# Performance work log

Hardware: AMD Instinct MI355X
Metric: run time of the kernel (lower is better)

The kernel has to match this reference:

```python
import jax, jax.numpy as jnp
import numpy as np

B, T, V = 128, 257, 1024   # T = U + 1 (structural constraint of the module)
U = 256
N_EMB, D_EMB = 1000, 512
NEG = -1e30
BLANK = 0


def setup_inputs() -> dict:
    key = jax.random.key(0)
    k0, k1, k2, k3, k4 = jax.random.split(key, 5)
    x = jax.random.normal(k0, (B, T, V), jnp.float32)
    y = jax.random.randint(k1, (B, U), 1, N_EMB, dtype=jnp.int32)  # labels in [1, 999], never blank
    xlen = jnp.full((B,), T, jnp.int32)
    ylen = jnp.full((B,), U, jnp.int32)
    embed_w = jax.random.normal(k2, (N_EMB, D_EMB), jnp.float32)
    lin_w = jax.random.normal(k3, (V, D_EMB), jnp.float32) / np.float32(np.sqrt(D_EMB))
    lin_b = jax.random.normal(k4, (V,), jnp.float32) * 0.01
    return {"x": x, "xlen": xlen, "y": y, "ylen": ylen,
            "embed_w": embed_w, "lin_w": lin_w, "lin_b": lin_b}


def _ctc_loss_sum(lp, targets, xlen, ylen):
    # lp: [T, B, V] treated as log-probs (faithful to the original, which feeds raw
    # logits straight into torch.nn.CTCLoss). targets: [B, U] padded with blank.
    Tn, Bn, _ = lp.shape
    Un = targets.shape[1]
    S = 2 * Un + 1
    # extended label sequence: blank, y1, blank, y2, ..., blank   -> [B, S]
    ext = jnp.full((Bn, S), BLANK, targets.dtype).at[:, 1::2].set(targets)
    bidx = jnp.arange(Bn)[:, None]
    lp_ext = lp[:, bidx, ext]                       # [T, B, S]
    # skip transition s-2 -> s allowed iff ext[s] != blank and ext[s] != ext[s-2]
    ext_m2 = jnp.pad(ext, ((0, 0), (2, 0)), constant_values=-1)[:, :S]
    skip_ok = (ext != BLANK) & (ext != ext_m2)      # [B, S]

    def lse3(a, b, c):
        m = jnp.maximum(jnp.maximum(a, b), c)
        return m + jnp.log(jnp.exp(a - m) + jnp.exp(b - m) + jnp.exp(c - m))

    alpha0 = (jnp.full((Bn, S), NEG, lp.dtype)
              .at[:, 0].set(lp_ext[0, :, 0])
              .at[:, 1].set(lp_ext[0, :, 1]))

    def step(alpha, lp_t):
        a1 = jnp.pad(alpha, ((0, 0), (1, 0)), constant_values=NEG)[:, :S]
        a2 = jnp.pad(alpha, ((0, 0), (2, 0)), constant_values=NEG)[:, :S]
        a2 = jnp.where(skip_ok, a2, NEG)
        new = lp_t + lse3(alpha, a1, a2)
        return new, new

    _, rest = jax.lax.scan(step, alpha0, lp_ext[1:])
    alphas = jnp.concatenate([alpha0[None], rest], axis=0)   # [T, B, S]
    aT = alphas[xlen - 1, jnp.arange(Bn)]                    # [B, S] at each seq's last frame
    s_last = 2 * ylen                                        # final blank position
    ll = jnp.logaddexp(aT[jnp.arange(Bn), s_last],
                       aT[jnp.arange(Bn), s_last - 1])
    return -jnp.sum(ll)                                      # reduction='sum'


def reference(x, xlen, y, ylen, embed_w, lin_w, lin_b):
    # mask padded label positions to blank (make_pad_mask + masked_fill_)
    pad = jnp.arange(y.shape[1], dtype=ylen.dtype)[None, :] >= ylen[:, None]
    y = jnp.where(pad, 0, y)
    z = jnp.concatenate([jnp.zeros((y.shape[0], 1), y.dtype), y], axis=1)  # [B, U+1]
    h = embed_w[z]                                   # [B, T, 512]
    logits = x + h @ lin_w.T + lin_b                 # [B, T, 1024]
    log_probs = jnp.transpose(logits, (1, 0, 2))     # [T, B, V]
    return _ctc_loss_sum(log_probs, y, xlen, ylen)
```

## Files before the change

kernel.cpp:

```cpp
#include <hip/hip_runtime.h>

#define NEG (-1e30f)

constexpr int B_ = 128;
constexpr int T_ = 257;
constexpr int V_ = 1024;
constexpr int U_ = 256;
constexpr int DE_ = 512;


__global__ __launch_bounds__(256) void gather_kernel(const float* __restrict__ x,
                                                     const int* __restrict__ y,
                                                     const int* __restrict__ ylen,
                                                     const float* __restrict__ E,
                                                     const float* __restrict__ L,
                                                     const float* __restrict__ bias,
                                                     float4* __restrict__ V)
{
    const int wave = (blockIdx.x << 2) | (threadIdx.x >> 6);
    if (wave >= B_ * T_) return;
    const int lane = threadIdx.x & 63;
    const int t = wave >> 7;
    const int b = wave & 127;

    const int yl = ylen[b];
    int ym1 = 0, yt = 0, ym2 = 0;
    if (t >= 1 && (t - 1) < yl) ym1 = y[b * U_ + t - 1];
    if (t <= 255 && t < yl)     yt  = y[b * U_ + t];
    if (t >= 2 && (t - 2) < yl) ym2 = y[b * U_ + t - 2];
    const int z = (t == 0) ? 0 : ym1;

    const float4* Ez = (const float4*)(E + (size_t)z * DE_);
    const float4* L0 = (const float4*)L;
    const float4* Lz = (const float4*)(L + (size_t)z * DE_);
    const float4* Lh = (const float4*)(L + (size_t)yt * DE_);
    float s_bl = 0.f, s_lo = 0.f, s_hi = 0.f;
    #pragma unroll
    for (int h = 0; h < 2; ++h) {
        const int idx = lane + h * 64;
        const float4 e = Ez[idx];
        const float4 l0 = L0[idx], lz = Lz[idx], lh = Lh[idx];
        s_bl += e.x * l0.x + e.y * l0.y + e.z * l0.z + e.w * l0.w;
        s_lo += e.x * lz.x + e.y * lz.y + e.z * lz.z + e.w * lz.w;
        s_hi += e.x * lh.x + e.y * lh.y + e.z * lh.z + e.w * lh.w;
    }
    #pragma unroll
    for (int m = 1; m < 64; m <<= 1) {
        s_bl += __shfl_xor(s_bl, m, 64);
        s_lo += __shfl_xor(s_lo, m, 64);
        s_hi += __shfl_xor(s_hi, m, 64);
    }

    if (lane == 0) {
        const float* xrow = x + ((size_t)b * T_ + t) * V_;
        const float v_bl = xrow[0] + s_bl + bias[0];
        const float v_lo = (t >= 1) ? (xrow[z] + s_lo + bias[z]) : NEG;
        const float v_hi = xrow[yt] + s_hi + bias[yt];
        int flags = 0;
        if (t >= 1 && t <= 255 && yt != 0 && yt != ym1) flags |= 1;
        if (t >= 2 && ym1 != 0 && ym1 != ym2)           flags |= 2;
        V[wave] = make_float4(v_lo, v_bl, v_hi, __int_as_float(flags));
    }
}

__global__ __launch_bounds__(128) void ctc_band_kernel(const float4* __restrict__ V,
                                                       float* __restrict__ out)
{
    const int tid = threadIdx.x;

    float4 ring[8];
    #pragma unroll
    for (int i = 0; i < 8; ++i) ring[i] = V[i * B_ + tid];

    float lo = NEG, mid = ring[0].y, hi = ring[0].z;
    ring[0] = V[8 * B_ + tid];

    for (int tb = 0; tb < 32; ++tb) {
        #pragma unroll
        for (int j = 1; j <= 8; ++j) {
            const int t = tb * 8 + j;
            const float4 f = ring[j & 7];
            if (t + 8 <= 256) ring[j & 7] = V[(size_t)(t + 8) * B_ + tid];
            const int flags = __float_as_int(f.w);
            const float nh = f.z + ((flags & 1) ? hi : NEG);
            const float nm = f.y + hi;
            const float a2 = (flags & 2) ? lo : NEG;
            const float m = fmaxf(fmaxf(hi, mid), a2);
            const float nl = f.x + m +
                __logf(__expf(hi - m) + __expf(mid - m) + __expf(a2 - m));
            hi = nh; mid = nm; lo = nl;
        }
    }
    const float mm = fmaxf(mid, lo);
    const float ll = mm + __logf(__expf(mid - mm) + __expf(lo - mm));

    __shared__ float sh[B_];
    sh[tid] = ll;
    __syncthreads();
    if (tid < 64) {
        float v = sh[tid] + sh[tid + 64];
        #pragma unroll
        for (int m = 1; m < 64; m <<= 1) v += __shfl_xor(v, m, 64);
        if (tid == 0) out[0] = -v;
    }
}

extern "C" void kernel_launch(void* const* d_in, const int* in_sizes, int n_in,
                              void* d_out, int out_size, void* d_ws, size_t ws_size,
                              hipStream_t stream)
{
    const float* x       = (const float*)d_in[0];
    const int*   y       = (const int*)  d_in[2];
    const int*   ylen    = (const int*)  d_in[3];
    const float* embed_w = (const float*)d_in[4];
    const float* lin_w   = (const float*)d_in[5];
    const float* lin_b   = (const float*)d_in[6];

    float4* V = (float4*)d_ws;
    float* out = (float*)d_out;

    const int n_tasks = B_ * T_;
    gather_kernel<<<dim3((n_tasks + 3) / 4), dim3(256), 0, stream>>>(
        x, y, ylen, embed_w, lin_w, lin_b, V);
    ctc_band_kernel<<<dim3(1), dim3(128), 0, stream>>>(V, out);
}
```

Baseline: 235.9 us.

## Fuse gather and CTC recursion into one kernel via last-block atomic counter

Merges the per-frame gather kernel and the single-block CTC alpha recursion into one launch. Each block bumps a global atomic counter after writing its results, and the last block to finish runs the serial band recursion and the final reduction. The x-row loads are also issued earlier, before the dot products. This removes one kernel launch and its inter-kernel gap, at the cost of a memset of the counter and a fence plus atomic in every block.

```diff
diff --git a/kernel.cpp b/kernel.cpp
--- a/kernel.cpp
+++ b/kernel.cpp
@@ -7,95 +7,111 @@
 constexpr int V_ = 1024;
 constexpr int U_ = 256;
 constexpr int DE_ = 512;
+constexpr int NWAVE_ = B_ * T_;
+constexpr int NBLK_ = (NWAVE_ + 3) / 4;
 
-
-__global__ __launch_bounds__(256) void gather_kernel(const float* __restrict__ x,
-                                                     const int* __restrict__ y,
-                                                     const int* __restrict__ ylen,
-                                                     const float* __restrict__ E,
-                                                     const float* __restrict__ L,
-                                                     const float* __restrict__ bias,
-                                                     float4* __restrict__ V)
+__global__ __launch_bounds__(256) void fused_ctc_kernel(const float* __restrict__ x,
+                                                        const int* __restrict__ y,
+                                                        const int* __restrict__ ylen,
+                                                        const float* __restrict__ E,
+                                                        const float* __restrict__ L,
+                                                        const float* __restrict__ bias,
+                                                        float4* __restrict__ V,
+                                                        unsigned* __restrict__ cnt,
+                                                        float* __restrict__ out)
 {
     const int wave = (blockIdx.x << 2) | (threadIdx.x >> 6);
-    if (wave >= B_ * T_) return;
     const int lane = threadIdx.x & 63;
-    const int t = wave >> 7;
-    const int b = wave & 127;
+    if (wave < NWAVE_) {
+        const int t = wave >> 7;
+        const int b = wave & 127;
 
-    const int yl = ylen[b];
-    int ym1 = 0, yt = 0, ym2 = 0;
-    if (t >= 1 && (t - 1) < yl) ym1 = y[b * U_ + t - 1];
-    if (t <= 255 && t < yl)     yt  = y[b * U_ + t];
-    if (t >= 2 && (t - 2) < yl) ym2 = y[b * U_ + t - 2];
-    const int z = (t == 0) ? 0 : ym1;
+        const int yl = ylen[b];
+        int ym1 = 0, yt = 0, ym2 = 0;
+        if (t >= 1 && (t - 1) < yl) ym1 = y[b * U_ + t - 1];
+        if (t <= 255 && t < yl)     yt  = y[b * U_ + t];
+        if (t >= 2 && (t - 2) < yl) ym2 = y[b * U_ + t - 2];
+        const int z = (t == 0) ? 0 : ym1;
 
-    const float4* Ez = (const float4*)(E + (size_t)z * DE_);
-    const float4* L0 = (const float4*)L;
-    const float4* Lz = (const float4*)(L + (size_t)z * DE_);
-    const float4* Lh = (const float4*)(L + (size_t)yt * DE_);
-    float s_bl = 0.f, s_lo = 0.f, s_hi = 0.f;
-    #pragma unroll
-    for (int h = 0; h < 2; ++h) {
-        const int idx = lane + h * 64;
-        const float4 e = Ez[idx];
-        const float4 l0 = L0[idx], lz = Lz[idx], lh = Lh[idx];
-        s_bl += e.x * l0.x + e.y * l0.y + e.z * l0.z + e.w * l0.w;
-        s_lo += e.x * lz.x + e.y * lz.y + e.z * lz.z + e.w * lz.w;
-        s_hi += e.x * lh.x + e.y * lh.y + e.z * lh.z + e.w * lh.w;
-    }
-    #pragma unroll
-    for (int m = 1; m < 64; m <<= 1) {
-        s_bl += __shfl_xor(s_bl, m, 64);
-        s_lo += __shfl_xor(s_lo, m, 64);
-        s_hi += __shfl_xor(s_hi, m, 64);
+        const float* xrow = x + ((size_t)b * T_ + t) * V_;
+        const float xb0 = xrow[0];
+        const float xbz = xrow[z];
+        const float xbh = xrow[yt];
+
+        const float4* Ez = (const float4*)(E + (size_t)z * DE_);
+        const float4* L0 = (const float4*)L;
+        const float4* Lz = (const float4*)(L + (size_t)z * DE_);
+        const float4* Lh = (const float4*)(L + (size_t)yt * DE_);
+        float s_bl = 0.f, s_lo = 0.f, s_hi = 0.f;
+        #pragma unroll
+        for (int h = 0; h < 2; ++h) {
+            const int idx = lane + h * 64;
+            const float4 e = Ez[idx];
+            const float4 l0 = L0[idx], lz = Lz[idx], lh = Lh[idx];
+            s_bl += e.x * l0.x + e.y * l0.y + e.z * l0.z + e.w * l0.w;
+            s_lo += e.x * lz.x + e.y * lz.y + e.z * lz.z + e.w * lz.w;
+            s_hi += e.x * lh.x + e.y * lh.y + e.z * lh.z + e.w * lh.w;
+        }
+        #pragma unroll
+        for (int m = 1; m < 64; m <<= 1) {
+            s_bl += __shfl_xor(s_bl, m, 64);
+            s_lo += __shfl_xor(s_lo, m, 64);
+            s_hi += __shfl_xor(s_hi, m, 64);
+        }
+
+        if (lane == 0) {
+            const float v_bl = xb0 + s_bl + bias[0];
+            const float v_lo = (t >= 1) ? (xbz + s_lo + bias[z]) : NEG;
+            const float v_hi = xbh + s_hi + bias[yt];
+            int flags = 0;
+            if (t >= 1 && t <= 255 && yt != 0 && yt != ym1) flags |= 1;
+            if (t >= 2 && ym1 != 0 && ym1 != ym2)           flags |= 2;
+            V[wave] = make_float4(v_lo, v_bl, v_hi, __int_as_float(flags));
+        }
     }
 
-    if (lane == 0) {
-        const float* xrow = x + ((size_t)b * T_ + t) * V_;
-        const float v_bl = xrow[0] + s_bl + bias[0];
-        const float v_lo = (t >= 1) ? (xrow[z] + s_lo + bias[z]) : NEG;
-        const float v_hi = xrow[yt] + s_hi + bias[yt];
-        int flags = 0;
-        if (t >= 1 && t <= 255 && yt != 0 && yt != ym1) flags |= 1;
-        if (t >= 2 && ym1 != 0 && ym1 != ym2)           flags |= 2;
-        V[wave] = make_float4(v_lo, v_bl, v_hi, __int_as_float(flags));
+    __shared__ int is_last;
+    __syncthreads();
+    if (threadIdx.x == 0) {
+        __threadfence();
+        is_last = (atomicAdd(cnt, 1u) == (unsigned)(NBLK_ - 1));
     }
-}
+    __syncthreads();
+    if (!is_last) return;
+    __threadfence();
 
-__global__ __launch_bounds__(128) void ctc_band_kernel(const float4* __restrict__ V,
-                                                       float* __restrict__ out)
-{
     const int tid = threadIdx.x;
+    float ll = 0.f;
+    if (tid < B_) {
+        float4 ring[8];
+        #pragma unroll
+        for (int i = 0; i < 8; ++i) ring[i] = V[i * B_ + tid];
 
-    float4 ring[8];
-    #pragma unroll
-    for (int i = 0; i < 8; ++i) ring[i] = V[i * B_ + tid];
+        float lo = NEG, mid = ring[0].y, hi = ring[0].z;
+        ring[0] = V[8 * B_ + tid];
 
-    float lo = NEG, mid = ring[0].y, hi = ring[0].z;
-    ring[0] = V[8 * B_ + tid];
-
-    for (int tb = 0; tb < 32; ++tb) {
-        #pragma unroll
-        for (int j = 1; j <= 8; ++j) {
-            const int t = tb * 8 + j;
-            const float4 f = ring[j & 7];
-            if (t + 8 <= 256) ring[j & 7] = V[(size_t)(t + 8) * B_ + tid];
-            const int flags = __float_as_int(f.w);
-            const float nh = f.z + ((flags & 1) ? hi : NEG);
-            const float nm = f.y + hi;
-            const float a2 = (flags & 2) ? lo : NEG;
-            const float m = fmaxf(fmaxf(hi, mid), a2);
-            const float nl = f.x + m +
-                __logf(__expf(hi - m) + __expf(mid - m) + __expf(a2 - m));
-            hi = nh; mid = nm; lo = nl;
+        for (int tb = 0; tb < 32; ++tb) {
+            #pragma unroll
+            for (int j = 1; j <= 8; ++j) {
+                const int t = tb * 8 + j;
+                const float4 f = ring[j & 7];
+                if (t + 8 <= 256) ring[j & 7] = V[(size_t)(t + 8) * B_ + tid];
+                const int flags = __float_as_int(f.w);
+                const float nh = f.z + ((flags & 1) ? hi : NEG);
+                const float nm = f.y + hi;
+                const float a2 = (flags & 2) ? lo : NEG;
+                const float m = fmaxf(fmaxf(hi, mid), a2);
+                const float nl = f.x + m +
+                    __logf(__expf(hi - m) + __expf(mid - m) + __expf(a2 - m));
+                hi = nh; mid = nm; lo = nl;
+            }
         }
+        const float mm = fmaxf(mid, lo);
+        ll = mm + __logf(__expf(mid - mm) + __expf(lo - mm));
     }
-    const float mm = fmaxf(mid, lo);
-    const float ll = mm + __logf(__expf(mid - mm) + __expf(lo - mm));
 
     __shared__ float sh[B_];
-    sh[tid] = ll;
+    if (tid < B_) sh[tid] = ll;
     __syncthreads();
     if (tid < 64) {
         float v = sh[tid] + sh[tid + 64];
@@ -116,11 +132,11 @@
     const float* lin_w   = (const float*)d_in[5];
     const float* lin_b   = (const float*)d_in[6];
 
-    float4* V = (float4*)d_ws;
-    float* out = (float*)d_out;
+    float4*   V   = (float4*)d_ws;
+    unsigned* cnt = (unsigned*)((char*)d_ws + (size_t)NWAVE_ * sizeof(float4));
+    float*    out = (float*)d_out;
 
-    const int n_tasks = B_ * T_;
-    gather_kernel<<<dim3((n_tasks + 3) / 4), dim3(256), 0, stream>>>(
-        x, y, ylen, embed_w, lin_w, lin_b, V);
-    ctc_band_kernel<<<dim3(1), dim3(128), 0, stream>>>(V, out);
+    hipMemsetAsync(cnt, 0, sizeof(unsigned), stream);
+    fused_ctc_kernel<<<dim3(NBLK_), dim3(256), 0, stream>>>(
+        x, y, ylen, embed_w, lin_w, lin_b, V, cnt, out);
 }
```

New measurement: 472.7 us. +100.3%, slower.

## Stream CTC scan inputs through LDS with async global_load_lds and hoist x loads

Applied to the files above, without the earlier changes.

The serial CTC scan kernel now prefetches per-timestep float4 records into a 4-slot LDS ring with global_load_lds, three chunks of 8 timesteps ahead, and waits with an explicit vmcnt. This replaces the 8-deep register ring, aiming to hide global latency on the single-block critical path. The gather kernel issues its x-row loads before the dot-product reduction so their latency overlaps the arithmetic. It also reads past T for padded chunks (up to t=282 rows), which may read beyond the written workspace region, though those values are unused.

```diff
diff --git a/kernel.cpp b/kernel.cpp
--- a/kernel.cpp
+++ b/kernel.cpp
@@ -7,6 +7,13 @@
 constexpr int V_ = 1024;
 constexpr int U_ = 256;
 constexpr int DE_ = 512;
+constexpr int NWAVE_ = B_ * T_;
+constexpr int TPAD_ = 280;
+
+#define GLOAD_LDS(g, l)                                                     \
+    __builtin_amdgcn_global_load_lds(                                       \
+        (const __attribute__((address_space(1))) void*)(g),                 \
+        (__attribute__((address_space(3))) void*)(l), 16, 0, 0)
 
 
 __global__ __launch_bounds__(256) void gather_kernel(const float* __restrict__ x,
@@ -18,7 +25,7 @@
                                                      float4* __restrict__ V)
 {
     const int wave = (blockIdx.x << 2) | (threadIdx.x >> 6);
-    if (wave >= B_ * T_) return;
+    if (wave >= NWAVE_) return;
     const int lane = threadIdx.x & 63;
     const int t = wave >> 7;
     const int b = wave & 127;
@@ -29,6 +36,11 @@
     if (t <= 255 && t < yl)     yt  = y[b * U_ + t];
     if (t >= 2 && (t - 2) < yl) ym2 = y[b * U_ + t - 2];
     const int z = (t == 0) ? 0 : ym1;
+
+    const float* xrow = x + ((size_t)b * T_ + t) * V_;
+    const float xb0 = xrow[0];
+    const float xbz = xrow[z];
+    const float xbh = xrow[yt];
 
     const float4* Ez = (const float4*)(E + (size_t)z * DE_);
     const float4* L0 = (const float4*)L;
@@ -52,10 +64,9 @@
     }
 
     if (lane == 0) {
-        const float* xrow = x + ((size_t)b * T_ + t) * V_;
-        const float v_bl = xrow[0] + s_bl + bias[0];
-        const float v_lo = (t >= 1) ? (xrow[z] + s_lo + bias[z]) : NEG;
-        const float v_hi = xrow[yt] + s_hi + bias[yt];
+        const float v_bl = xb0 + s_bl + bias[0];
+        const float v_lo = (t >= 1) ? (xbz + s_lo + bias[z]) : NEG;
+        const float v_hi = xbh + s_hi + bias[yt];
         int flags = 0;
         if (t >= 1 && t <= 255 && yt != 0 && yt != ym1) flags |= 1;
         if (t >= 2 && ym1 != 0 && ym1 != ym2)           flags |= 2;
@@ -63,46 +74,75 @@
     }
 }
 
-__global__ __launch_bounds__(128) void ctc_band_kernel(const float4* __restrict__ V,
+__global__ __launch_bounds__(128) void ctc_scan_kernel(const float4* __restrict__ V,
                                                        float* __restrict__ out)
 {
+    __shared__ __align__(16) float buf[2][4][8][256];
     const int tid = threadIdx.x;
+    const int w = tid >> 6;
+    const int lane = tid & 63;
 
-    float4 ring[8];
+    const float4* gbase = V + w * 64 + lane;
+
     #pragma unroll
-    for (int i = 0; i < 8; ++i) ring[i] = V[i * B_ + tid];
+    for (int c = 0; c < 3; ++c)
+        #pragma unroll
+        for (int r = 0; r < 8; ++r)
+            GLOAD_LDS(gbase + (size_t)(c * 8 + r) * B_, &buf[w][c][r][0]);
 
-    float lo = NEG, mid = ring[0].y, hi = ring[0].z;
-    ring[0] = V[8 * B_ + tid];
+    asm volatile("s_waitcnt vmcnt(16)" ::: "memory");
 
-    for (int tb = 0; tb < 32; ++tb) {
+    float lo = NEG, mid, hi;
+    {
+        const float4 f = *(const float4*)&buf[w][0][0][lane * 4];
+        mid = f.y; hi = f.z;
+    }
+    #pragma unroll
+    for (int r = 1; r < 8; ++r) {
+        const float4 f = *(const float4*)&buf[w][0][r][lane * 4];
+        const int flags = __float_as_int(f.w);
+        const float nh = f.z + ((flags & 1) ? hi : NEG);
+        const float nm = f.y + hi;
+        const float a2 = (flags & 2) ? lo : NEG;
+        const float m = fmaxf(fmaxf(hi, mid), a2);
+        const float nl = f.x + m +
+            __logf(__expf(hi - m) + __expf(mid - m) + __expf(a2 - m));
+        hi = nh; mid = nm; lo = nl;
+    }
+
+    for (int c = 1; c <= 32; ++c) {
+        const int snew = (c + 2) & 3;
         #pragma unroll
-        for (int j = 1; j <= 8; ++j) {
-            const int t = tb * 8 + j;
-            const float4 f = ring[j & 7];
-            if (t + 8 <= 256) ring[j & 7] = V[(size_t)(t + 8) * B_ + tid];
-            const int flags = __float_as_int(f.w);
-            const float nh = f.z + ((flags & 1) ? hi : NEG);
-            const float nm = f.y + hi;
-            const float a2 = (flags & 2) ? lo : NEG;
-            const float m = fmaxf(fmaxf(hi, mid), a2);
-            const float nl = f.x + m +
-                __logf(__expf(hi - m) + __expf(mid - m) + __expf(a2 - m));
-            hi = nh; mid = nm; lo = nl;
+        for (int r = 0; r < 8; ++r)
+            GLOAD_LDS(gbase + (size_t)((c + 2) * 8 + r) * B_, &buf[w][snew][r][0]);
+        asm volatile("s_waitcnt vmcnt(16)" ::: "memory");
+        const int slot = c & 3;
+        #pragma unroll
+        for (int r = 0; r < 8; ++r) {
+            const int t = c * 8 + r;
+            if (t <= 256) {
+                const float4 f = *(const float4*)&buf[w][slot][r][lane * 4];
+                const int flags = __float_as_int(f.w);
+                const float nh = f.z + ((flags & 1) ? hi : NEG);
+                const float nm = f.y + hi;
+                const float a2 = (flags & 2) ? lo : NEG;
+                const float m = fmaxf(fmaxf(hi, mid), a2);
+                const float nl = f.x + m +
+                    __logf(__expf(hi - m) + __expf(mid - m) + __expf(a2 - m));
+                hi = nh; mid = nm; lo = nl;
+            }
         }
     }
+
     const float mm = fmaxf(mid, lo);
-    const float ll = mm + __logf(__expf(mid - mm) + __expf(lo - mm));
+    float ll = mm + __logf(__expf(mid - mm) + __expf(lo - mm));
+    #pragma unroll
+    for (int m = 1; m < 64; m <<= 1) ll += __shfl_xor(ll, m, 64);
 
-    __shared__ float sh[B_];
-    sh[tid] = ll;
     __syncthreads();
-    if (tid < 64) {
-        float v = sh[tid] + sh[tid + 64];
-        #pragma unroll
-        for (int m = 1; m < 64; m <<= 1) v += __shfl_xor(v, m, 64);
-        if (tid == 0) out[0] = -v;
-    }
+    if (lane == 0) ((volatile float*)buf)[w] = ll;
+    __syncthreads();
+    if (tid == 0) out[0] = -(((volatile float*)buf)[0] + ((volatile float*)buf)[1]);
 }
 
 extern "C" void kernel_launch(void* const* d_in, const int* in_sizes, int n_in,
@@ -116,11 +156,11 @@
     const float* lin_w   = (const float*)d_in[5];
     const float* lin_b   = (const float*)d_in[6];
 
-    float4* V = (float4*)d_ws;
+    float4* V  = (float4*)d_ws;
     float* out = (float*)d_out;
 
-    const int n_tasks = B_ * T_;
-    gather_kernel<<<dim3((n_tasks + 3) / 4), dim3(256), 0, stream>>>(
+    const int nblk = (NWAVE_ + 3) / 4;
+    gather_kernel<<<dim3(nblk), dim3(256), 0, stream>>>(
         x, y, ylen, embed_w, lin_w, lin_b, V);
-    ctc_band_kernel<<<dim3(1), dim3(128), 0, stream>>>(V, out);
+    ctc_scan_kernel<<<dim3(1), dim3(128), 0, stream>>>(V, out);
 }
```

After: 228.8 us. 1.03x faster.

## Split CTC scan across eight blocks with LDS staging and atomic reduction

Applied to the files above, without the earlier changes.

Splits the serial CTC recurrence from one 128-thread block into eight blocks, each handling 16 batch items. The gather kernel now writes in a group-major layout so each block can bulk-load its 256 timesteps into shared memory before a 16-lane scan reads them from LDS instead of global memory. The per-group partial sums are combined with an atomicAdd onto an output zeroed by a memset. The x-row loads are also issued before the dot products to overlap their latency. This spreads the latency-bound scan over more compute units, at the cost of an extra memset launch and a nondeterministic float summation order.

```diff
diff --git a/kernel.cpp b/kernel.cpp
--- a/kernel.cpp
+++ b/kernel.cpp
@@ -7,6 +7,7 @@
 constexpr int V_ = 1024;
 constexpr int U_ = 256;
 constexpr int DE_ = 512;
+constexpr int NWAVE_ = B_ * T_;
 
 
 __global__ __launch_bounds__(256) void gather_kernel(const float* __restrict__ x,
@@ -18,7 +19,7 @@
                                                      float4* __restrict__ V)
 {
     const int wave = (blockIdx.x << 2) | (threadIdx.x >> 6);
-    if (wave >= B_ * T_) return;
+    if (wave >= NWAVE_) return;
     const int lane = threadIdx.x & 63;
     const int t = wave >> 7;
     const int b = wave & 127;
@@ -29,6 +30,11 @@
     if (t <= 255 && t < yl)     yt  = y[b * U_ + t];
     if (t >= 2 && (t - 2) < yl) ym2 = y[b * U_ + t - 2];
     const int z = (t == 0) ? 0 : ym1;
+
+    const float* xrow = x + ((size_t)b * T_ + t) * V_;
+    const float xb0 = xrow[0];
+    const float xbz = xrow[z];
+    const float xbh = xrow[yt];
 
     const float4* Ez = (const float4*)(E + (size_t)z * DE_);
     const float4* L0 = (const float4*)L;
@@ -52,35 +58,39 @@
     }
 
     if (lane == 0) {
-        const float* xrow = x + ((size_t)b * T_ + t) * V_;
-        const float v_bl = xrow[0] + s_bl + bias[0];
-        const float v_lo = (t >= 1) ? (xrow[z] + s_lo + bias[z]) : NEG;
-        const float v_hi = xrow[yt] + s_hi + bias[yt];
+        const float v_bl = xb0 + s_bl + bias[0];
+        const float v_lo = (t >= 1) ? (xbz + s_lo + bias[z]) : NEG;
+        const float v_hi = xbh + s_hi + bias[yt];
         int flags = 0;
         if (t >= 1 && t <= 255 && yt != 0 && yt != ym1) flags |= 1;
         if (t >= 2 && ym1 != 0 && ym1 != ym2)           flags |= 2;
-        V[wave] = make_float4(v_lo, v_bl, v_hi, __int_as_float(flags));
+        const int g = b >> 4, j = b & 15;
+        V[((size_t)(g * 257 + t) << 4) + j] =
+            make_float4(v_lo, v_bl, v_hi, __int_as_float(flags));
     }
 }
 
-__global__ __launch_bounds__(128) void ctc_band_kernel(const float4* __restrict__ V,
+__global__ __launch_bounds__(256) void ctc_scan_kernel(const float4* __restrict__ V,
                                                        float* __restrict__ out)
 {
+    __shared__ __align__(16) float4 buf[256][16];
     const int tid = threadIdx.x;
+    const int g = blockIdx.x;
+    const float4* Vg = V + (size_t)g * 257 * 16;
 
-    float4 ring[8];
     #pragma unroll
-    for (int i = 0; i < 8; ++i) ring[i] = V[i * B_ + tid];
+    for (int k = 0; k < 16; ++k) {
+        const int idx = tid + k * 256;
+        ((float4*)buf)[idx] = Vg[16 + idx];
+    }
+    __syncthreads();
 
-    float lo = NEG, mid = ring[0].y, hi = ring[0].z;
-    ring[0] = V[8 * B_ + tid];
-
-    for (int tb = 0; tb < 32; ++tb) {
-        #pragma unroll
-        for (int j = 1; j <= 8; ++j) {
-            const int t = tb * 8 + j;
-            const float4 f = ring[j & 7];
-            if (t + 8 <= 256) ring[j & 7] = V[(size_t)(t + 8) * B_ + tid];
+    if (tid < 16) {
+        const float4 f0 = Vg[tid];
+        float lo = NEG, mid = f0.y, hi = f0.z;
+        #pragma unroll 8
+        for (int t = 1; t <= 256; ++t) {
+            const float4 f = buf[t - 1][tid];
             const int flags = __float_as_int(f.w);
             const float nh = f.z + ((flags & 1) ? hi : NEG);
             const float nm = f.y + hi;
@@ -90,18 +100,11 @@
                 __logf(__expf(hi - m) + __expf(mid - m) + __expf(a2 - m));
             hi = nh; mid = nm; lo = nl;
         }
-    }
-    const float mm = fmaxf(mid, lo);
-    const float ll = mm + __logf(__expf(mid - mm) + __expf(lo - mm));
-
-    __shared__ float sh[B_];
-    sh[tid] = ll;
-    __syncthreads();
-    if (tid < 64) {
-        float v = sh[tid] + sh[tid + 64];
+        const float mm = fmaxf(mid, lo);
+        float ll = mm + __logf(__expf(mid - mm) + __expf(lo - mm));
         #pragma unroll
-        for (int m = 1; m < 64; m <<= 1) v += __shfl_xor(v, m, 64);
-        if (tid == 0) out[0] = -v;
+        for (int m = 1; m < 16; m <<= 1) ll += __shfl_xor(ll, m, 64);
+        if (tid == 0) atomicAdd(out, -ll);
     }
 }
 
@@ -116,11 +119,12 @@
     const float* lin_w   = (const float*)d_in[5];
     const float* lin_b   = (const float*)d_in[6];
 
-    float4* V = (float4*)d_ws;
+    float4* V  = (float4*)d_ws;
     float* out = (float*)d_out;
 
-    const int n_tasks = B_ * T_;
-    gather_kernel<<<dim3((n_tasks + 3) / 4), dim3(256), 0, stream>>>(
+    hipMemsetAsync(out, 0, sizeof(float), stream);
+    const int nblk = (NWAVE_ + 3) / 4;
+    gather_kernel<<<dim3(nblk), dim3(256), 0, stream>>>(
         x, y, ylen, embed_w, lin_w, lin_b, V);
-    ctc_band_kernel<<<dim3(1), dim3(128), 0, stream>>>(V, out);
+    ctc_scan_kernel<<<dim3(8), dim3(256), 0, stream>>>(V, out);
 }
```

After: 224.1 us. 5.0% less time.
